# Kernel tuning notes

Hardware: AMD Instinct MI355X
Metric: run time of the kernel (lower is better)

The kernel has to match this reference:

```python
import jax, jax.numpy as jnp
import numpy as np

B, N, E = 65536, 5, 8
NF, EF = 7, 2            # raw node/edge feature dims
D, DE = 128, 32          # node/edge embedding dims
L = 4                    # num_convs
PD = 256                 # pool_dim
M1, M2 = 256, 64         # MLP hidden sizes
NEG_SLOPE = 0.01


def lrelu(x):
    return jnp.where(x >= 0, x, NEG_SLOPE * x)


def setup_inputs() -> dict:
    key = jax.random.key(0)
    ks = iter(jax.random.split(key, 40))

    def w(shape, scale=0.05):
        return (jax.random.normal(next(ks), shape, dtype=jnp.float32) * scale)

    inp = {
        "node_feat": jax.random.normal(next(ks), (B, N, NF), dtype=jnp.float32),
        "edge_feat": jax.random.normal(next(ks), (B, E, EF), dtype=jnp.float32),
        "edge_index": jax.random.randint(next(ks), (2, E), 0, N, dtype=jnp.int64),
        "node_w": w((NF, D)), "node_b": jnp.zeros((D,), jnp.float32),
        "edge_w": w((EF, DE)), "edge_b": jnp.zeros((DE,), jnp.float32),
        # stacked per-conv params (L layers)
        "msg_w1": w((L, 2 * D + DE, D)), "msg_b1": jnp.zeros((L, D), jnp.float32),
        "msg_w2": w((L, D, D)), "msg_b2": jnp.zeros((L, D), jnp.float32),
        "upd_w1": w((L, 2 * D, D)), "upd_b1": jnp.zeros((L, D), jnp.float32),
        "upd_g1": jnp.ones((L, N), jnp.float32), "upd_be1": jnp.zeros((L, N), jnp.float32),
        "upd_w2": w((L, D, D)), "upd_b2": jnp.zeros((L, D), jnp.float32),
        "upd_g2": jnp.ones((L, N), jnp.float32), "upd_be2": jnp.zeros((L, N), jnp.float32),
        "pool_w": w((N * D, PD)), "pool_b": jnp.zeros((PD,), jnp.float32),
        "pool_g": jnp.ones((PD,), jnp.float32), "pool_be": jnp.zeros((PD,), jnp.float32),
        "mlp1_w": w((PD, M1)), "mlp1_b": jnp.zeros((M1,), jnp.float32),
        "mlp1_g": jnp.ones((M1,), jnp.float32), "mlp1_be": jnp.zeros((M1,), jnp.float32),
        "mlp2_w": w((M1, M2)), "mlp2_b": jnp.zeros((M2,), jnp.float32),
        "mlp2_g": jnp.ones((M2,), jnp.float32), "mlp2_be": jnp.zeros((M2,), jnp.float32),
    }
    return inp


def _forward(node_feat, edge_feat, edge_index,
             node_w, node_b, edge_w, edge_b,
             msg_w1, msg_b1, msg_w2, msg_b2,
             upd_w1, upd_b1, upd_g1, upd_be1,
             upd_w2, upd_b2, upd_g2, upd_be2,
             pool_w, pool_b, pool_g, pool_be,
             mlp1_w, mlp1_b, mlp1_g, mlp1_be,
             mlp2_w, mlp2_b, mlp2_g, mlp2_be):
    src, dst = edge_index[0], edge_index[1]  # PyG: row0 = j (source), row1 = i (target)
    x = node_feat @ node_w + node_b                    # [B,N,D]
    ea = edge_feat @ edge_w + edge_b                   # [B,E,DE]
    for l in range(L):
        h_i = x[:, dst, :]                             # [B,E,D]
        h_j = x[:, src, :]
        m = jnp.concatenate([h_i, h_j, ea], axis=-1)   # [B,E,2D+DE]
        m = lrelu(m @ msg_w1[l] + msg_b1[l])
        m = lrelu(m @ msg_w2[l] + msg_b2[l])           # [B,E,D]
        agg = jnp.zeros_like(x).at[:, dst, :].add(m)   # scatter-add over nodes
        u = jnp.concatenate([x, agg], axis=-1)         # [B,N,2D]
        u = u @ upd_w1[l] + upd_b1[l]
        u = u * upd_g1[l][None, :, None] + upd_be1[l][None, :, None]  # BatchNorm1d(5), eval
        u = lrelu(u)
        u = u @ upd_w2[l] + upd_b2[l]
        u = u * upd_g2[l][None, :, None] + upd_be2[l][None, :, None]
        u = lrelu(u)
        x = x + u                                      # residual
    p = x.reshape(B, N * D)                            # == cat([x[:,i,:] for i in range(5)])
    p = lrelu((p @ pool_w + pool_b) * pool_g + pool_be)
    p = lrelu((p @ mlp1_w + mlp1_b) * mlp1_g + mlp1_be)
    p = lrelu((p @ mlp2_w + mlp2_b) * mlp2_g + mlp2_be)
    return jnp.mean(p, axis=-1)                        # AvgPool1d over final dim -> [B]


def reference(node_feat, edge_feat, edge_index,
              node_w, node_b, edge_w, edge_b,
              msg_w1, msg_b1, msg_w2, msg_b2,
              upd_w1, upd_b1, upd_g1, upd_be1,
              upd_w2, upd_b2, upd_g2, upd_be2,
              pool_w, pool_b, pool_g, pool_be,
              mlp1_w, mlp1_b, mlp1_g, mlp1_be,
              mlp2_w, mlp2_b, mlp2_g, mlp2_be):
    return _forward(node_feat, edge_feat, edge_index,
                    node_w, node_b, edge_w, edge_b,
                    msg_w1, msg_b1, msg_w2, msg_b2,
                    upd_w1, upd_b1, upd_g1, upd_be1,
                    upd_w2, upd_b2, upd_g2, upd_be2,
                    pool_w, pool_b, pool_g, pool_be,
                    mlp1_w, mlp1_b, mlp1_g, mlp1_be,
                    mlp2_w, mlp2_b, mlp2_g, mlp2_be)
```

## Files before the change

### kernel.cpp

```cpp
#include <hip/hip_runtime.h>


typedef _Float16 h8 __attribute__((ext_vector_type(8)));
typedef float f4 __attribute__((ext_vector_type(4)));

constexpr int NB = 65536;
constexpr int GG = 8;
constexpr int NBLK = NB / GG;

__device__ __forceinline__ float lrelu(float v){ return v >= 0.f ? v : 0.01f*v; }
__device__ __forceinline__ int div5(int v){ return (v*52429)>>18; }

__device__ __forceinline__ _Float16* sw8(char* base, int row, int offh){
    int byte = (row<<8) + (offh<<1);
    byte ^= (row&7)<<4;
    return (_Float16*)(base + byte);
}
__device__ __forceinline__ _Float16* swea(char* base, int row, int offh){
    int byte = (row<<6) + (offh<<1);
    byte ^= (row&3)<<4;
    return (_Float16*)(base + byte);
}

#define MFMA(a,b,c) __builtin_amdgcn_mfma_f32_16x16x32_f16((a),(b),(c),0,0,0)

__device__ __forceinline__ f4 z4(){ f4 v; v[0]=0.f; v[1]=0.f; v[2]=0.f; v[3]=0.f; return v; }

__global__ void prep_t(const float* __restrict__ src, _Float16* __restrict__ dst,
                       int K, int N, int total){
    int i = blockIdx.x*256 + threadIdx.x;
    if (i >= total) return;
    int kn = K*N;
    int l = i / kn; int r = i - l*kn;
    int n = r / K;  int k = r - n*K;
    dst[i] = (_Float16)src[(size_t)l*kn + (size_t)k*N + n];
}

constexpr int O_MSG1 = 0;
constexpr int O_MSG2 = 147456;
constexpr int O_UPD1 = 212992;
constexpr int O_UPD2 = 344064;
constexpr int O_POOL = 409600;
constexpr int O_MLP1 = 573440;
constexpr int O_MLP2 = 638976;

constexpr int LO_XH  = 0;
constexpr int LO_EA  = 12288;
constexpr int LO_BUF = 16384;
constexpr int LO_AGG = 32768;
constexpr int LDS_BYTES = 45056;

__global__ __launch_bounds__(256)
void gnn_mfma(const float* __restrict__ nfeat, const float* __restrict__ efeat,
              const int* __restrict__ eidx,
              const float* __restrict__ node_w, const float* __restrict__ node_b,
              const float* __restrict__ edge_w, const float* __restrict__ edge_b,
              const _Float16* __restrict__ wT,
              const float* __restrict__ msg_b1, const float* __restrict__ msg_b2,
              const float* __restrict__ upd_b1, const float* __restrict__ upd_g1, const float* __restrict__ upd_be1,
              const float* __restrict__ upd_b2, const float* __restrict__ upd_g2, const float* __restrict__ upd_be2,
              const float* __restrict__ pool_b, const float* __restrict__ pool_g, const float* __restrict__ pool_be,
              const float* __restrict__ mlp1_b, const float* __restrict__ mlp1_g, const float* __restrict__ mlp1_be,
              const float* __restrict__ mlp2_b, const float* __restrict__ mlp2_g, const float* __restrict__ mlp2_be,
              float* __restrict__ out)
{
    __shared__ __align__(16) char smem[LDS_BYTES];
    char* xh  = smem + LO_XH;
    char* ea  = smem + LO_EA;
    char* buf = smem + LO_BUF;
    char* agg = smem + LO_AGG;
    float* miscf = (float*)(smem + LO_AGG);
    float* partf = (float*)(smem + LO_AGG);

    const int tid  = threadIdx.x;
    const int w    = tid >> 6;
    const int lane = tid & 63;
    const int l15  = lane & 15;
    const int kg   = lane >> 4;
    const int mgM  = w >> 1;
    const int ngM  = w & 1;
    const int mgU  = w >> 1;
    const int cntU = (mgU == 0) ? 2 : 1;
    const int gbase = blockIdx.x * GG;

    int dp = 0, sp = 0;
    {
        bool is64 = true;
        #pragma unroll
        for (int i = 1; i < 16; i += 2) if (eidx[i] != 0) is64 = false;
        #pragma unroll
        for (int e = 0; e < 8; ++e){
            int s = is64 ? eidx[2*e]     : eidx[e];
            int d = is64 ? eidx[16+2*e]  : eidx[8+e];
            sp |= s << (4*e); dp |= d << (4*e);
        }
    }
    const int eMine = l15 & 7;
    const int myDst = (dp >> (4*eMine)) & 15;
    const int mySrc = (sp >> (4*eMine)) & 15;

    for (int i = tid; i < 408; i += 256){
        if (i < 280) miscf[i] = nfeat[(size_t)gbase*35 + i];
        else         miscf[i] = efeat[(size_t)gbase*16 + (i - 280)];
    }
    __syncthreads();

    {
        int ge = tid >> 2, c8 = (tid & 3) * 8;
        int g  = ge >> 3, e = ge & 7;
        float f0 = miscf[280 + g*16 + e*2];
        float f1 = miscf[280 + g*16 + e*2 + 1];
        h8 v;
        #pragma unroll
        for (int j = 0; j < 8; ++j){
            int c = c8 + j;
            v[j] = (_Float16)(edge_b[c] + f0*edge_w[c] + f1*edge_w[32 + c]);
        }
        *(h8*)swea(ea, ge, c8) = v;
    }

    float xreg[2][4][4];
    #pragma unroll
    for (int mi = 0; mi < 2; ++mi){
        if (mi < cntU){
            int mt = mgU*2 + mi;
            #pragma unroll
            for (int nt = 0; nt < 4; ++nt){
                int col = ngM*64 + nt*16 + l15;
                float w0 = node_w[0*128+col], w1 = node_w[1*128+col],
                      w2 = node_w[2*128+col], w3 = node_w[3*128+col],
                      w4 = node_w[4*128+col], w5 = node_w[5*128+col],
                      w6 = node_w[6*128+col];
                float bb = node_b[col];
                #pragma unroll
                for (int r = 0; r < 4; ++r){
                    int row = mt*16 + kg*4 + r;
                    int g = div5(row), n = row - 5*g;
                    const float* nf = &miscf[g*35 + n*7];
                    float v = bb + nf[0]*w0 + nf[1]*w1 + nf[2]*w2 + nf[3]*w3
                                 + nf[4]*w4 + nf[5]*w5 + nf[6]*w6;
                    xreg[mi][nt][r] = v;
                    if (row < 40) *sw8(xh, row, col) = (_Float16)v;
                }
            }
        }
    }
    __syncthreads();

    for (int l = 0; l < 4; ++l){
        const _Float16* W1 = wT + O_MSG1 + (size_t)l*36864;
        const _Float16* W2 = wT + O_MSG2 + (size_t)l*16384;
        const _Float16* W3 = wT + O_UPD1 + (size_t)l*32768;
        const _Float16* W4 = wT + O_UPD2 + (size_t)l*16384;

        {
            f4 acc[2][4];
            #pragma unroll
            for (int mi=0;mi<2;++mi){ acc[mi][0]=z4(); acc[mi][1]=z4(); acc[mi][2]=z4(); acc[mi][3]=z4(); }
            int xrow_d[2], xrow_s[2], earow[2];
            #pragma unroll
            for (int mi = 0; mi < 2; ++mi){
                int mt = mgM*2 + mi;
                int g  = mt*2 + (l15 >> 3);
                xrow_d[mi] = g*5 + myDst;
                xrow_s[mi] = g*5 + mySrc;
                earow[mi]  = mt*16 + l15;
            }
            const _Float16* Bp = W1 + (size_t)(ngM*64 + l15)*288 + kg*8;
            #pragma unroll
            for (int kc = 0; kc < 4; ++kc){
                h8 a0 = *(const h8*)sw8(xh, xrow_d[0], kc*32 + kg*8);
                h8 a1 = *(const h8*)sw8(xh, xrow_d[1], kc*32 + kg*8);
                #pragma unroll
                for (int np = 0; np < 2; ++np){
                    h8 b0 = *(const h8*)(Bp + (2*np+0)*4608 + kc*32);
                    h8 b1 = *(const h8*)(Bp + (2*np+1)*4608 + kc*32);
                    acc[0][2*np]=MFMA(a0,b0,acc[0][2*np]); acc[0][2*np+1]=MFMA(a0,b1,acc[0][2*np+1]);
                    acc[1][2*np]=MFMA(a1,b0,acc[1][2*np]); acc[1][2*np+1]=MFMA(a1,b1,acc[1][2*np+1]);
                }
            }
            #pragma unroll
            for (int kc = 0; kc < 4; ++kc){
                h8 a0 = *(const h8*)sw8(xh, xrow_s[0], kc*32 + kg*8);
                h8 a1 = *(const h8*)sw8(xh, xrow_s[1], kc*32 + kg*8);
                #pragma unroll
                for (int np = 0; np < 2; ++np){
                    h8 b0 = *(const h8*)(Bp + (2*np+0)*4608 + 128 + kc*32);
                    h8 b1 = *(const h8*)(Bp + (2*np+1)*4608 + 128 + kc*32);
                    acc[0][2*np]=MFMA(a0,b0,acc[0][2*np]); acc[0][2*np+1]=MFMA(a0,b1,acc[0][2*np+1]);
                    acc[1][2*np]=MFMA(a1,b0,acc[1][2*np]); acc[1][2*np+1]=MFMA(a1,b1,acc[1][2*np+1]);
                }
            }
            {
                h8 a0 = *(const h8*)swea(ea, earow[0], kg*8);
                h8 a1 = *(const h8*)swea(ea, earow[1], kg*8);
                #pragma unroll
                for (int np = 0; np < 2; ++np){
                    h8 b0 = *(const h8*)(Bp + (2*np+0)*4608 + 256);
                    h8 b1 = *(const h8*)(Bp + (2*np+1)*4608 + 256);
                    acc[0][2*np]=MFMA(a0,b0,acc[0][2*np]); acc[0][2*np+1]=MFMA(a0,b1,acc[0][2*np+1]);
                    acc[1][2*np]=MFMA(a1,b0,acc[1][2*np]); acc[1][2*np+1]=MFMA(a1,b1,acc[1][2*np+1]);
                }
            }
            #pragma unroll
            for (int mi = 0; mi < 2; ++mi){
                int mt = mgM*2 + mi;
                #pragma unroll
                for (int nt = 0; nt < 4; ++nt){
                    int col = ngM*64 + nt*16 + l15;
                    float bb = msg_b1[l*128 + col];
                    #pragma unroll
                    for (int r = 0; r < 4; ++r){
                        int row = mt*16 + kg*4 + r;
                        *sw8(buf, row, col) = (_Float16)lrelu(acc[mi][nt][r] + bb);
                    }
                }
            }
        }
        __syncthreads();

        {
            f4 acc[2][4];
            #pragma unroll
            for (int mi=0;mi<2;++mi){ acc[mi][0]=z4(); acc[mi][1]=z4(); acc[mi][2]=z4(); acc[mi][3]=z4(); }
            const _Float16* Bp = W2 + (size_t)(ngM*64 + l15)*128 + kg*8;
            #pragma unroll
            for (int kc = 0; kc < 4; ++kc){
                h8 a0 = *(const h8*)sw8(buf, (mgM*2+0)*16 + l15, kc*32 + kg*8);
                h8 a1 = *(const h8*)sw8(buf, (mgM*2+1)*16 + l15, kc*32 + kg*8);
                #pragma unroll
                for (int np = 0; np < 2; ++np){
                    h8 b0 = *(const h8*)(Bp + (2*np+0)*2048 + kc*32);
                    h8 b1 = *(const h8*)(Bp + (2*np+1)*2048 + kc*32);
                    acc[0][2*np]=MFMA(a0,b0,acc[0][2*np]); acc[0][2*np+1]=MFMA(a0,b1,acc[0][2*np+1]);
                    acc[1][2*np]=MFMA(a1,b0,acc[1][2*np]); acc[1][2*np+1]=MFMA(a1,b1,acc[1][2*np+1]);
                }
            }
            __syncthreads();
            #pragma unroll
            for (int mi = 0; mi < 2; ++mi){
                int mt = mgM*2 + mi;
                #pragma unroll
                for (int nt = 0; nt < 4; ++nt){
                    int col = ngM*64 + nt*16 + l15;
                    float bb = msg_b2[l*128 + col];
                    #pragma unroll
                    for (int r = 0; r < 4; ++r){
                        int row = mt*16 + kg*4 + r;
                        *sw8(buf, row, col) = (_Float16)lrelu(acc[mi][nt][r] + bb);
                    }
                }
            }
        }
        __syncthreads();

        for (int u = tid; u < 640; u += 256){
            int gn = u >> 4, c8 = (u & 15)*8;
            int g = div5(gn), n = gn - 5*g;
            float s0=0,s1=0,s2=0,s3=0,s4=0,s5=0,s6=0,s7=0;
            #pragma unroll
            for (int e = 0; e < 8; ++e){
                if (((dp >> (4*e)) & 15) == n){
                    h8 v = *(const h8*)sw8(buf, g*8 + e, c8);
                    s0+=(float)v[0]; s1+=(float)v[1]; s2+=(float)v[2]; s3+=(float)v[3];
                    s4+=(float)v[4]; s5+=(float)v[5]; s6+=(float)v[6]; s7+=(float)v[7];
                }
            }
            h8 o;
            o[0]=(_Float16)s0; o[1]=(_Float16)s1; o[2]=(_Float16)s2; o[3]=(_Float16)s3;
            o[4]=(_Float16)s4; o[5]=(_Float16)s5; o[6]=(_Float16)s6; o[7]=(_Float16)s7;
            *(h8*)sw8(agg, gn, c8) = o;
        }
        __syncthreads();

        {
            f4 acc[2][4];
            #pragma unroll
            for (int mi=0;mi<2;++mi){ acc[mi][0]=z4(); acc[mi][1]=z4(); acc[mi][2]=z4(); acc[mi][3]=z4(); }
            const _Float16* Bp = W3 + (size_t)(ngM*64 + l15)*256 + kg*8;
            #pragma unroll
            for (int kc = 0; kc < 8; ++kc){
                h8 a0, a1;
                if (kc < 4) { a0 = *(const h8*)sw8(xh,  (mgU*2+0)*16 + l15, kc*32 + kg*8); }
                else        { a0 = *(const h8*)sw8(agg, (mgU*2+0)*16 + l15, (kc-4)*32 + kg*8); }
                if (cntU > 1){
                    if (kc < 4) { a1 = *(const h8*)sw8(xh,  (mgU*2+1)*16 + l15, kc*32 + kg*8); }
                    else        { a1 = *(const h8*)sw8(agg, (mgU*2+1)*16 + l15, (kc-4)*32 + kg*8); }
                } else a1 = a0;
                #pragma unroll
                for (int np = 0; np < 2; ++np){
                    h8 b0 = *(const h8*)(Bp + (2*np+0)*4096 + kc*32);
                    h8 b1 = *(const h8*)(Bp + (2*np+1)*4096 + kc*32);
                    acc[0][2*np]=MFMA(a0,b0,acc[0][2*np]); acc[0][2*np+1]=MFMA(a0,b1,acc[0][2*np+1]);
                    if (cntU > 1){
                        acc[1][2*np]=MFMA(a1,b0,acc[1][2*np]); acc[1][2*np+1]=MFMA(a1,b1,acc[1][2*np+1]);
                    }
                }
            }
            #pragma unroll
            for (int mi = 0; mi < 2; ++mi){
                if (mi < cntU){
                    int mt = mgU*2 + mi;
                    #pragma unroll
                    for (int nt = 0; nt < 4; ++nt){
                        int col = ngM*64 + nt*16 + l15;
                        float bb = upd_b1[l*128 + col];
                        #pragma unroll
                        for (int r = 0; r < 4; ++r){
                            int crow = mt*16 + kg*4 + r;
                            if (crow < 40){
                                int n = crow - 5*div5(crow);
                                float val = lrelu((acc[mi][nt][r] + bb)*upd_g1[l*5+n] + upd_be1[l*5+n]);
                                *sw8(buf, crow, col) = (_Float16)val;
                            }
                        }
                    }
                }
            }
        }
        __syncthreads();

        {
            f4 acc[2][4];
            #pragma unroll
            for (int mi=0;mi<2;++mi){ acc[mi][0]=z4(); acc[mi][1]=z4(); acc[mi][2]=z4(); acc[mi][3]=z4(); }
            const _Float16* Bp = W4 + (size_t)(ngM*64 + l15)*128 + kg*8;
            #pragma unroll
            for (int kc = 0; kc < 4; ++kc){
                h8 a0 = *(const h8*)sw8(buf, (mgU*2+0)*16 + l15, kc*32 + kg*8);
                h8 a1 = (cntU > 1) ? *(const h8*)sw8(buf, (mgU*2+1)*16 + l15, kc*32 + kg*8) : a0;
                #pragma unroll
                for (int np = 0; np < 2; ++np){
                    h8 b0 = *(const h8*)(Bp + (2*np+0)*2048 + kc*32);
                    h8 b1 = *(const h8*)(Bp + (2*np+1)*2048 + kc*32);
                    acc[0][2*np]=MFMA(a0,b0,acc[0][2*np]); acc[0][2*np+1]=MFMA(a0,b1,acc[0][2*np+1]);
                    if (cntU > 1){
                        acc[1][2*np]=MFMA(a1,b0,acc[1][2*np]); acc[1][2*np+1]=MFMA(a1,b1,acc[1][2*np+1]);
                    }
                }
            }
            #pragma unroll
            for (int mi = 0; mi < 2; ++mi){
                if (mi < cntU){
                    int mt = mgU*2 + mi;
                    #pragma unroll
                    for (int nt = 0; nt < 4; ++nt){
                        int col = ngM*64 + nt*16 + l15;
                        float bb = upd_b2[l*128 + col];
                        #pragma unroll
                        for (int r = 0; r < 4; ++r){
                            int crow = mt*16 + kg*4 + r;
                            int n = crow - 5*div5(crow);
                            float val = lrelu((acc[mi][nt][r] + bb)*upd_g2[l*5+n] + upd_be2[l*5+n]);
                            xreg[mi][nt][r] += val;
                            if (crow < 40) *sw8(xh, crow, col) = (_Float16)xreg[mi][nt][r];
                        }
                    }
                }
            }
        }
        __syncthreads();
    }

    {
        f4 accP[4];
        #pragma unroll
        for (int nt=0;nt<4;++nt) accP[nt]=z4();
        const _Float16* Bp = wT + O_POOL + (size_t)(w*64 + l15)*640 + kg*8;
        #pragma unroll
        for (int kc = 0; kc < 20; ++kc){
            int k0 = kc*32 + kg*8;
            int n  = k0 >> 7, d = k0 & 127;
            h8 a  = *(const h8*)sw8(xh, (l15 & 7)*5 + n, d);
            #pragma unroll
            for (int nt = 0; nt < 4; ++nt){
                h8 b = *(const h8*)(Bp + nt*10240 + kc*32);
                accP[nt] = MFMA(a, b, accP[nt]);
            }
        }
        #pragma unroll
        for (int nt = 0; nt < 4; ++nt){
            int col = w*64 + nt*16 + l15;
            float pb = pool_b[col], pg = pool_g[col], pe = pool_be[col];
            #pragma unroll
            for (int r = 0; r < 4; ++r){
                int g = kg*4 + r;
                if (g < 8){
                    float val = lrelu((accP[nt][r] + pb)*pg + pe);
                    int prow = g + 16*(col >> 7);
                    *sw8(buf, prow, col & 127) = (_Float16)val;
                }
            }
        }
    }
    __syncthreads();

    {
        f4 accQ[4];
        #pragma unroll
        for (int nt=0;nt<4;++nt) accQ[nt]=z4();
        const _Float16* Bp = wT + O_MLP1 + (size_t)(w*64 + l15)*256 + kg*8;
        #pragma unroll
        for (int kc = 0; kc < 8; ++kc){
            int k0 = kc*32 + kg*8;
            int arow = (l15 & 7) + 16*(k0 >> 7);
            h8 a = *(const h8*)sw8(buf, arow, k0 & 127);
            #pragma unroll
            for (int nt = 0; nt < 4; ++nt){
                h8 b = *(const h8*)(Bp + nt*4096 + kc*32);
                accQ[nt] = MFMA(a, b, accQ[nt]);
            }
        }
        __syncthreads();
        #pragma unroll
        for (int nt = 0; nt < 4; ++nt){
            int col = w*64 + nt*16 + l15;
            float qb = mlp1_b[col], qg = mlp1_g[col], qe = mlp1_be[col];
            #pragma unroll
            for (int r = 0; r < 4; ++r){
                int g = kg*4 + r;
                if (g < 8){
                    float val = lrelu((accQ[nt][r] + qb)*qg + qe);
                    int qrow = 32 + g + 16*(col >> 7);
                    *sw8(buf, qrow, col & 127) = (_Float16)val;
                }
            }
        }
    }
    __syncthreads();

    {
        f4 accR = z4();
        const _Float16* Bp = wT + O_MLP2 + (size_t)(w*16 + l15)*256 + kg*8;
        #pragma unroll
        for (int kc = 0; kc < 8; ++kc){
            int k0 = kc*32 + kg*8;
            int arow = 32 + (l15 & 7) + 16*(k0 >> 7);
            h8 a = *(const h8*)sw8(buf, arow, k0 & 127);
            h8 b = *(const h8*)(Bp + kc*32);
            accR = MFMA(a, b, accR);
        }
        int col = w*16 + l15;
        float rb = mlp2_b[col], rg = mlp2_g[col], re = mlp2_be[col];
        #pragma unroll
        for (int r = 0; r < 4; ++r){
            float val = lrelu((accR[r] + rb)*rg + re);
            val += __shfl_xor(val, 1);
            val += __shfl_xor(val, 2);
            val += __shfl_xor(val, 4);
            val += __shfl_xor(val, 8);
            if (l15 == 0) partf[w*16 + (kg*4 + r)] = val;
        }
    }
    __syncthreads();
    if (tid < 8){
        float s = partf[tid] + partf[16+tid] + partf[32+tid] + partf[48+tid];
        out[gbase + tid] = s * (1.0f/64.0f);
    }
}

extern "C" void kernel_launch(void* const* d_in, const int* in_sizes, int n_in,
                              void* d_out, int out_size, void* d_ws, size_t ws_size,
                              hipStream_t stream) {
    _Float16* wT = (_Float16*)d_ws;
    auto T = [&](const void* src, int dstoff, int L, int K, int N){
        int total = L*K*N;
        prep_t<<<(total + 255)/256, 256, 0, stream>>>((const float*)src, wT + dstoff, K, N, total);
    };
    T(d_in[7],  O_MSG1, 4, 288, 128);
    T(d_in[9],  O_MSG2, 4, 128, 128);
    T(d_in[11], O_UPD1, 4, 256, 128);
    T(d_in[15], O_UPD2, 4, 128, 128);
    T(d_in[19], O_POOL, 1, 640, 256);
    T(d_in[23], O_MLP1, 1, 256, 256);
    T(d_in[27], O_MLP2, 1, 256, 64);

    gnn_mfma<<<NBLK, 256, 0, stream>>>(
        (const float*)d_in[0], (const float*)d_in[1], (const int*)d_in[2],
        (const float*)d_in[3], (const float*)d_in[4],
        (const float*)d_in[5], (const float*)d_in[6],
        wT,
        (const float*)d_in[8],  (const float*)d_in[10],
        (const float*)d_in[12], (const float*)d_in[13], (const float*)d_in[14],
        (const float*)d_in[16], (const float*)d_in[17], (const float*)d_in[18],
        (const float*)d_in[20], (const float*)d_in[21], (const float*)d_in[22],
        (const float*)d_in[24], (const float*)d_in[25], (const float*)d_in[26],
        (const float*)d_in[28], (const float*)d_in[29], (const float*)d_in[30],
        (float*)d_out);
}
```

Before: 2.182 ms.

## Give each wave two whole graphs to remove block barriers in conv layers

Each wave now owns two graphs (10 node rows, 16 edge rows) and computes all 128 output columns itself, where before the 4 waves split M and N tiles of the whole 8-graph block. This removes every __syncthreads inside the 4 conv layers and the feature-load barrier, keeping only one barrier before pooling. In exchange every wave loads all 8 B-tiles per k-chunk, doubling weight traffic per wave. Padded MFMA rows are also wasted in the node-side GEMMs (10 valid of 16 rows).

```diff
diff --git a/kernel.cpp b/kernel.cpp
--- a/kernel.cpp
+++ b/kernel.cpp
@@ -9,7 +9,6 @@
 constexpr int NBLK = NB / GG;
 
 __device__ __forceinline__ float lrelu(float v){ return v >= 0.f ? v : 0.01f*v; }
-__device__ __forceinline__ int div5(int v){ return (v*52429)>>18; }
 
 __device__ __forceinline__ _Float16* sw8(char* base, int row, int offh){
     int byte = (row<<8) + (offh<<1);
@@ -69,7 +68,6 @@
     char* ea  = smem + LO_EA;
     char* buf = smem + LO_BUF;
     char* agg = smem + LO_AGG;
-    float* miscf = (float*)(smem + LO_AGG);
     float* partf = (float*)(smem + LO_AGG);
 
     const int tid  = threadIdx.x;
@@ -77,11 +75,9 @@
     const int lane = tid & 63;
     const int l15  = lane & 15;
     const int kg   = lane >> 4;
-    const int mgM  = w >> 1;
-    const int ngM  = w & 1;
-    const int mgU  = w >> 1;
-    const int cntU = (mgU == 0) ? 2 : 1;
     const int gbase = blockIdx.x * GG;
+    const int nrow0 = w * 10;
+    const int erow0 = w * 16;
 
     int dp = 0, sp = 0;
     {
@@ -99,53 +95,54 @@
     const int myDst = (dp >> (4*eMine)) & 15;
     const int mySrc = (sp >> (4*eMine)) & 15;
 
-    for (int i = tid; i < 408; i += 256){
-        if (i < 280) miscf[i] = nfeat[(size_t)gbase*35 + i];
-        else         miscf[i] = efeat[(size_t)gbase*16 + (i - 280)];
-    }
-    __syncthreads();
-
-    {
-        int ge = tid >> 2, c8 = (tid & 3) * 8;
-        int g  = ge >> 3, e = ge & 7;
-        float f0 = miscf[280 + g*16 + e*2];
-        float f1 = miscf[280 + g*16 + e*2 + 1];
+    float* misc = (float*)(agg + w*2560);
+    {
+        int gp = gbase + 2*w;
+        const float* nfp = nfeat + (size_t)gp*35;
+        misc[lane] = nfp[lane];
+        if (lane < 6)  misc[64 + lane] = nfp[64 + lane];
+        if (lane < 32) misc[70 + lane] = efeat[(size_t)gp*16 + lane];
+    }
+
+    {
+        int er = lane >> 2, c8 = (lane & 3) * 8;
+        int gl = er >> 3, e = er & 7;
+        float f0 = misc[70 + gl*16 + e*2];
+        float f1 = misc[70 + gl*16 + e*2 + 1];
         h8 v;
         #pragma unroll
         for (int j = 0; j < 8; ++j){
             int c = c8 + j;
             v[j] = (_Float16)(edge_b[c] + f0*edge_w[c] + f1*edge_w[32 + c]);
         }
-        *(h8*)swea(ea, ge, c8) = v;
-    }
-
-    float xreg[2][4][4];
+        *(h8*)swea(ea, erow0 + er, c8) = v;
+    }
+
+    float xreg[8][4];
     #pragma unroll
-    for (int mi = 0; mi < 2; ++mi){
-        if (mi < cntU){
-            int mt = mgU*2 + mi;
-            #pragma unroll
-            for (int nt = 0; nt < 4; ++nt){
-                int col = ngM*64 + nt*16 + l15;
-                float w0 = node_w[0*128+col], w1 = node_w[1*128+col],
-                      w2 = node_w[2*128+col], w3 = node_w[3*128+col],
-                      w4 = node_w[4*128+col], w5 = node_w[5*128+col],
-                      w6 = node_w[6*128+col];
-                float bb = node_b[col];
-                #pragma unroll
-                for (int r = 0; r < 4; ++r){
-                    int row = mt*16 + kg*4 + r;
-                    int g = div5(row), n = row - 5*g;
-                    const float* nf = &miscf[g*35 + n*7];
-                    float v = bb + nf[0]*w0 + nf[1]*w1 + nf[2]*w2 + nf[3]*w3
-                                 + nf[4]*w4 + nf[5]*w5 + nf[6]*w6;
-                    xreg[mi][nt][r] = v;
-                    if (row < 40) *sw8(xh, row, col) = (_Float16)v;
-                }
-            }
-        }
-    }
-    __syncthreads();
+    for (int nt = 0; nt < 8; ++nt){
+        int col = nt*16 + l15;
+        float w0 = node_w[0*128+col], w1 = node_w[1*128+col],
+              w2 = node_w[2*128+col], w3 = node_w[3*128+col],
+              w4 = node_w[4*128+col], w5 = node_w[5*128+col],
+              w6 = node_w[6*128+col];
+        float bb = node_b[col];
+        #pragma unroll
+        for (int r = 0; r < 4; ++r){
+            int v = kg*4 + r;
+            if (v < 10){
+                int gl = (v >= 5) ? 1 : 0;
+                int n  = v - 5*gl;
+                const float* nf = &misc[gl*35 + n*7];
+                float x = bb + nf[0]*w0 + nf[1]*w1 + nf[2]*w2 + nf[3]*w3
+                             + nf[4]*w4 + nf[5]*w5 + nf[6]*w6;
+                xreg[nt][r] = x;
+                *sw8(xh, nrow0 + v, col) = (_Float16)x;
+            } else {
+                xreg[nt][r] = 0.f;
+            }
+        }
+    }
 
     for (int l = 0; l < 4; ++l){
         const _Float16* W1 = wT + O_MSG1 + (size_t)l*36864;
@@ -154,114 +151,82 @@
         const _Float16* W4 = wT + O_UPD2 + (size_t)l*16384;
 
         {
-            f4 acc[2][4];
-            #pragma unroll
-            for (int mi=0;mi<2;++mi){ acc[mi][0]=z4(); acc[mi][1]=z4(); acc[mi][2]=z4(); acc[mi][3]=z4(); }
-            int xrow_d[2], xrow_s[2], earow[2];
-            #pragma unroll
-            for (int mi = 0; mi < 2; ++mi){
-                int mt = mgM*2 + mi;
-                int g  = mt*2 + (l15 >> 3);
-                xrow_d[mi] = g*5 + myDst;
-                xrow_s[mi] = g*5 + mySrc;
-                earow[mi]  = mt*16 + l15;
-            }
-            const _Float16* Bp = W1 + (size_t)(ngM*64 + l15)*288 + kg*8;
+            f4 acc[8];
+            #pragma unroll
+            for (int nt=0;nt<8;++nt) acc[nt]=z4();
+            int gp   = l15 >> 3;
+            int xrd  = nrow0 + gp*5 + myDst;
+            int xrs  = nrow0 + gp*5 + mySrc;
+            const _Float16* Bp = W1 + (size_t)l15*288 + kg*8;
             #pragma unroll
             for (int kc = 0; kc < 4; ++kc){
-                h8 a0 = *(const h8*)sw8(xh, xrow_d[0], kc*32 + kg*8);
-                h8 a1 = *(const h8*)sw8(xh, xrow_d[1], kc*32 + kg*8);
-                #pragma unroll
-                for (int np = 0; np < 2; ++np){
-                    h8 b0 = *(const h8*)(Bp + (2*np+0)*4608 + kc*32);
-                    h8 b1 = *(const h8*)(Bp + (2*np+1)*4608 + kc*32);
-                    acc[0][2*np]=MFMA(a0,b0,acc[0][2*np]); acc[0][2*np+1]=MFMA(a0,b1,acc[0][2*np+1]);
-                    acc[1][2*np]=MFMA(a1,b0,acc[1][2*np]); acc[1][2*np+1]=MFMA(a1,b1,acc[1][2*np+1]);
+                h8 a = *(const h8*)sw8(xh, xrd, kc*32 + kg*8);
+                #pragma unroll
+                for (int nt = 0; nt < 8; ++nt){
+                    h8 b = *(const h8*)(Bp + nt*4608 + kc*32);
+                    acc[nt] = MFMA(a, b, acc[nt]);
                 }
             }
             #pragma unroll
             for (int kc = 0; kc < 4; ++kc){
-                h8 a0 = *(const h8*)sw8(xh, xrow_s[0], kc*32 + kg*8);
-                h8 a1 = *(const h8*)sw8(xh, xrow_s[1], kc*32 + kg*8);
-                #pragma unroll
-                for (int np = 0; np < 2; ++np){
-                    h8 b0 = *(const h8*)(Bp + (2*np+0)*4608 + 128 + kc*32);
-                    h8 b1 = *(const h8*)(Bp + (2*np+1)*4608 + 128 + kc*32);
-                    acc[0][2*np]=MFMA(a0,b0,acc[0][2*np]); acc[0][2*np+1]=MFMA(a0,b1,acc[0][2*np+1]);
-                    acc[1][2*np]=MFMA(a1,b0,acc[1][2*np]); acc[1][2*np+1]=MFMA(a1,b1,acc[1][2*np+1]);
+                h8 a = *(const h8*)sw8(xh, xrs, kc*32 + kg*8);
+                #pragma unroll
+                for (int nt = 0; nt < 8; ++nt){
+                    h8 b = *(const h8*)(Bp + nt*4608 + 128 + kc*32);
+                    acc[nt] = MFMA(a, b, acc[nt]);
                 }
             }
             {
-                h8 a0 = *(const h8*)swea(ea, earow[0], kg*8);
-                h8 a1 = *(const h8*)swea(ea, earow[1], kg*8);
-                #pragma unroll
-                for (int np = 0; np < 2; ++np){
-                    h8 b0 = *(const h8*)(Bp + (2*np+0)*4608 + 256);
-                    h8 b1 = *(const h8*)(Bp + (2*np+1)*4608 + 256);
-                    acc[0][2*np]=MFMA(a0,b0,acc[0][2*np]); acc[0][2*np+1]=MFMA(a0,b1,acc[0][2*np+1]);
-                    acc[1][2*np]=MFMA(a1,b0,acc[1][2*np]); acc[1][2*np+1]=MFMA(a1,b1,acc[1][2*np+1]);
-                }
-            }
-            #pragma unroll
-            for (int mi = 0; mi < 2; ++mi){
-                int mt = mgM*2 + mi;
-                #pragma unroll
-                for (int nt = 0; nt < 4; ++nt){
-                    int col = ngM*64 + nt*16 + l15;
-                    float bb = msg_b1[l*128 + col];
-                    #pragma unroll
-                    for (int r = 0; r < 4; ++r){
-                        int row = mt*16 + kg*4 + r;
-                        *sw8(buf, row, col) = (_Float16)lrelu(acc[mi][nt][r] + bb);
-                    }
-                }
-            }
-        }
-        __syncthreads();
+                h8 a = *(const h8*)swea(ea, erow0 + l15, kg*8);
+                #pragma unroll
+                for (int nt = 0; nt < 8; ++nt){
+                    h8 b = *(const h8*)(Bp + nt*4608 + 256);
+                    acc[nt] = MFMA(a, b, acc[nt]);
+                }
+            }
+            #pragma unroll
+            for (int nt = 0; nt < 8; ++nt){
+                int col = nt*16 + l15;
+                float bb = msg_b1[l*128 + col];
+                #pragma unroll
+                for (int r = 0; r < 4; ++r)
+                    *sw8(buf, erow0 + kg*4 + r, col) = (_Float16)lrelu(acc[nt][r] + bb);
+            }
+        }
 
         {
-            f4 acc[2][4];
-            #pragma unroll
-            for (int mi=0;mi<2;++mi){ acc[mi][0]=z4(); acc[mi][1]=z4(); acc[mi][2]=z4(); acc[mi][3]=z4(); }
-            const _Float16* Bp = W2 + (size_t)(ngM*64 + l15)*128 + kg*8;
+            f4 acc[8];
+            #pragma unroll
+            for (int nt=0;nt<8;++nt) acc[nt]=z4();
+            const _Float16* Bp = W2 + (size_t)l15*128 + kg*8;
             #pragma unroll
             for (int kc = 0; kc < 4; ++kc){
-                h8 a0 = *(const h8*)sw8(buf, (mgM*2+0)*16 + l15, kc*32 + kg*8);
-                h8 a1 = *(const h8*)sw8(buf, (mgM*2+1)*16 + l15, kc*32 + kg*8);
-                #pragma unroll
-                for (int np = 0; np < 2; ++np){
-                    h8 b0 = *(const h8*)(Bp + (2*np+0)*2048 + kc*32);
-                    h8 b1 = *(const h8*)(Bp + (2*np+1)*2048 + kc*32);
-                    acc[0][2*np]=MFMA(a0,b0,acc[0][2*np]); acc[0][2*np+1]=MFMA(a0,b1,acc[0][2*np+1]);
-                    acc[1][2*np]=MFMA(a1,b0,acc[1][2*np]); acc[1][2*np+1]=MFMA(a1,b1,acc[1][2*np+1]);
-                }
-            }
-            __syncthreads();
-            #pragma unroll
-            for (int mi = 0; mi < 2; ++mi){
-                int mt = mgM*2 + mi;
-                #pragma unroll
-                for (int nt = 0; nt < 4; ++nt){
-                    int col = ngM*64 + nt*16 + l15;
-                    float bb = msg_b2[l*128 + col];
-                    #pragma unroll
-                    for (int r = 0; r < 4; ++r){
-                        int row = mt*16 + kg*4 + r;
-                        *sw8(buf, row, col) = (_Float16)lrelu(acc[mi][nt][r] + bb);
-                    }
-                }
-            }
-        }
-        __syncthreads();
-
-        for (int u = tid; u < 640; u += 256){
-            int gn = u >> 4, c8 = (u & 15)*8;
-            int g = div5(gn), n = gn - 5*g;
+                h8 a = *(const h8*)sw8(buf, erow0 + l15, kc*32 + kg*8);
+                #pragma unroll
+                for (int nt = 0; nt < 8; ++nt){
+                    h8 b = *(const h8*)(Bp + nt*2048 + kc*32);
+                    acc[nt] = MFMA(a, b, acc[nt]);
+                }
+            }
+            #pragma unroll
+            for (int nt = 0; nt < 8; ++nt){
+                int col = nt*16 + l15;
+                float bb = msg_b2[l*128 + col];
+                #pragma unroll
+                for (int r = 0; r < 4; ++r)
+                    *sw8(buf, erow0 + kg*4 + r, col) = (_Float16)lrelu(acc[nt][r] + bb);
+            }
+        }
+
+        for (int u = lane; u < 160; u += 64){
+            int idx = u >> 4, c8 = (u & 15)*8;
+            int gl = (idx >= 5) ? 1 : 0;
+            int n  = idx - 5*gl;
             float s0=0,s1=0,s2=0,s3=0,s4=0,s5=0,s6=0,s7=0;
             #pragma unroll
             for (int e = 0; e < 8; ++e){
                 if (((dp >> (4*e)) & 15) == n){
-                    h8 v = *(const h8*)sw8(buf, g*8 + e, c8);
+                    h8 v = *(const h8*)sw8(buf, erow0 + gl*8 + e, c8);
                     s0+=(float)v[0]; s1+=(float)v[1]; s2+=(float)v[2]; s3+=(float)v[3];
                     s4+=(float)v[4]; s5+=(float)v[5]; s6+=(float)v[6]; s7+=(float)v[7];
                 }
@@ -269,98 +234,74 @@
             h8 o;
             o[0]=(_Float16)s0; o[1]=(_Float16)s1; o[2]=(_Float16)s2; o[3]=(_Float16)s3;
             o[4]=(_Float16)s4; o[5]=(_Float16)s5; o[6]=(_Float16)s6; o[7]=(_Float16)s7;
-            *(h8*)sw8(agg, gn, c8) = o;
-        }
-        __syncthreads();
+            *(h8*)sw8(agg, nrow0 + idx, c8) = o;
+        }
 
         {
-            f4 acc[2][4];
-            #pragma unroll
-            for (int mi=0;mi<2;++mi){ acc[mi][0]=z4(); acc[mi][1]=z4(); acc[mi][2]=z4(); acc[mi][3]=z4(); }
-            const _Float16* Bp = W3 + (size_t)(ngM*64 + l15)*256 + kg*8;
+            f4 acc[8];
+            #pragma unroll
+            for (int nt=0;nt<8;++nt) acc[nt]=z4();
+            int arow = nrow0 + l15;
+            const _Float16* Bp = W3 + (size_t)l15*256 + kg*8;
             #pragma unroll
             for (int kc = 0; kc < 8; ++kc){
-                h8 a0, a1;
-                if (kc < 4) { a0 = *(const h8*)sw8(xh,  (mgU*2+0)*16 + l15, kc*32 + kg*8); }
-                else        { a0 = *(const h8*)sw8(agg, (mgU*2+0)*16 + l15, (kc-4)*32 + kg*8); }
-                if (cntU > 1){
-                    if (kc < 4) { a1 = *(const h8*)sw8(xh,  (mgU*2+1)*16 + l15, kc*32 + kg*8); }
-                    else        { a1 = *(const h8*)sw8(agg, (mgU*2+1)*16 + l15, (kc-4)*32 + kg*8); }
-                } else a1 = a0;
-                #pragma unroll
-                for (int np = 0; np < 2; ++np){
-                    h8 b0 = *(const h8*)(Bp + (2*np+0)*4096 + kc*32);
-                    h8 b1 = *(const h8*)(Bp + (2*np+1)*4096 + kc*32);
-                    acc[0][2*np]=MFMA(a0,b0,acc[0][2*np]); acc[0][2*np+1]=MFMA(a0,b1,acc[0][2*np+1]);
-                    if (cntU > 1){
-                        acc[1][2*np]=MFMA(a1,b0,acc[1][2*np]); acc[1][2*np+1]=MFMA(a1,b1,acc[1][2*np+1]);
+                h8 a = (kc < 4) ? *(const h8*)sw8(xh,  arow, kc*32 + kg*8)
+                                : *(const h8*)sw8(agg, arow, (kc-4)*32 + kg*8);
+                #pragma unroll
+                for (int nt = 0; nt < 8; ++nt){
+                    h8 b = *(const h8*)(Bp + nt*4096 + kc*32);
+                    acc[nt] = MFMA(a, b, acc[nt]);
+                }
+            }
+            #pragma unroll
+            for (int nt = 0; nt < 8; ++nt){
+                int col = nt*16 + l15;
+                float bb = upd_b1[l*128 + col];
+                #pragma unroll
+                for (int r = 0; r < 4; ++r){
+                    int v = kg*4 + r;
+                    if (v < 10){
+                        int n = v - ((v >= 5) ? 5 : 0);
+                        float val = lrelu((acc[nt][r] + bb)*upd_g1[l*5+n] + upd_be1[l*5+n]);
+                        *sw8(buf, erow0 + v, col) = (_Float16)val;
                     }
                 }
             }
-            #pragma unroll
-            for (int mi = 0; mi < 2; ++mi){
-                if (mi < cntU){
-                    int mt = mgU*2 + mi;
-                    #pragma unroll
-                    for (int nt = 0; nt < 4; ++nt){
-                        int col = ngM*64 + nt*16 + l15;
-                        float bb = upd_b1[l*128 + col];
-                        #pragma unroll
-                        for (int r = 0; r < 4; ++r){
-                            int crow = mt*16 + kg*4 + r;
-                            if (crow < 40){
-                                int n = crow - 5*div5(crow);
-                                float val = lrelu((acc[mi][nt][r] + bb)*upd_g1[l*5+n] + upd_be1[l*5+n]);
-                                *sw8(buf, crow, col) = (_Float16)val;
-                            }
-                        }
+        }
+
+        {
+            f4 acc[8];
+            #pragma unroll
+            for (int nt=0;nt<8;++nt) acc[nt]=z4();
+            const _Float16* Bp = W4 + (size_t)l15*128 + kg*8;
+            #pragma unroll
+            for (int kc = 0; kc < 4; ++kc){
+                h8 a = *(const h8*)sw8(buf, erow0 + l15, kc*32 + kg*8);
+                #pragma unroll
+                for (int nt = 0; nt < 8; ++nt){
+                    h8 b = *(const h8*)(Bp + nt*2048 + kc*32);
+                    acc[nt] = MFMA(a, b, acc[nt]);
+                }
+            }
+            #pragma unroll
+            for (int nt = 0; nt < 8; ++nt){
+                int col = nt*16 + l15;
+                float bb = upd_b2[l*128 + col];
+                #pragma unroll
+                for (int r = 0; r < 4; ++r){
+                    int v = kg*4 + r;
+                    if (v < 10){
+                        int n = v - ((v >= 5) ? 5 : 0);
+                        float val = lrelu((acc[nt][r] + bb)*upd_g2[l*5+n] + upd_be2[l*5+n]);
+                        xreg[nt][r] += val;
+                        *sw8(xh, nrow0 + v, col) = (_Float16)xreg[nt][r];
                     }
                 }
             }
         }
-        __syncthreads();
-
-        {
-            f4 acc[2][4];
-            #pragma unroll
-            for (int mi=0;mi<2;++mi){ acc[mi][0]=z4(); acc[mi][1]=z4(); acc[mi][2]=z4(); acc[mi][3]=z4(); }
-            const _Float16* Bp = W4 + (size_t)(ngM*64 + l15)*128 + kg*8;
-            #pragma unroll
-            for (int kc = 0; kc < 4; ++kc){
-                h8 a0 = *(const h8*)sw8(buf, (mgU*2+0)*16 + l15, kc*32 + kg*8);
-                h8 a1 = (cntU > 1) ? *(const h8*)sw8(buf, (mgU*2+1)*16 + l15, kc*32 + kg*8) : a0;
-                #pragma unroll
-                for (int np = 0; np < 2; ++np){
-                    h8 b0 = *(const h8*)(Bp + (2*np+0)*2048 + kc*32);
-                    h8 b1 = *(const h8*)(Bp + (2*np+1)*2048 + kc*32);
-                    acc[0][2*np]=MFMA(a0,b0,acc[0][2*np]); acc[0][2*np+1]=MFMA(a0,b1,acc[0][2*np+1]);
-                    if (cntU > 1){
-                        acc[1][2*np]=MFMA(a1,b0,acc[1][2*np]); acc[1][2*np+1]=MFMA(a1,b1,acc[1][2*np+1]);
-                    }
-                }
-            }
-            #pragma unroll
-            for (int mi = 0; mi < 2; ++mi){
-                if (mi < cntU){
-                    int mt = mgU*2 + mi;
-                    #pragma unroll
-                    for (int nt = 0; nt < 4; ++nt){
-                        int col = ngM*64 + nt*16 + l15;
-                        float bb = upd_b2[l*128 + col];
-                        #pragma unroll
-                        for (int r = 0; r < 4; ++r){
-                            int crow = mt*16 + kg*4 + r;
-                            int n = crow - 5*div5(crow);
-                            float val = lrelu((acc[mi][nt][r] + bb)*upd_g2[l*5+n] + upd_be2[l*5+n]);
-                            xreg[mi][nt][r] += val;
-                            if (crow < 40) *sw8(xh, crow, col) = (_Float16)xreg[mi][nt][r];
-                        }
-                    }
-                }
-            }
-        }
-        __syncthreads();
-    }
+    }
+
+    __syncthreads();
 
     {
         f4 accP[4];
```

New measurement: 4.845 ms. 122% more time.
